# Kernel tuning notes

Hardware: AMD Instinct MI355X
Metric: run time of the kernel (lower is better)

Reference implementation:

```python
import jax, jax.numpy as jnp
import numpy as np

D_MODEL = 1024
N_HEADS = 16
D_K = D_MODEL // N_HEADS  # 64
D_V = D_MODEL // N_HEADS  # 64
BATCH = 2
SEQ = 2048


def setup_inputs() -> dict:
    key = jax.random.key(0)
    k_x, k_q, k_k, k_v, k_o = jax.random.split(key, 5)
    s = 1.0 / np.sqrt(D_MODEL)
    return {
        "X": jax.random.normal(k_x, (BATCH, SEQ, D_MODEL), dtype=jnp.float32),
        "W_Q": jax.random.normal(k_q, (D_MODEL, N_HEADS * D_K), dtype=jnp.float32) * s,
        "W_K": jax.random.normal(k_k, (D_MODEL, N_HEADS * D_K), dtype=jnp.float32) * s,
        "W_V": jax.random.normal(k_v, (D_MODEL, N_HEADS * D_V), dtype=jnp.float32) * s,
        "W_0": jax.random.normal(k_o, (N_HEADS * D_V, D_MODEL), dtype=jnp.float32) * s,
    }


def reference(X, W_Q, W_K, W_V, W_0):
    B, S, _ = X.shape
    # Project and split heads: [B, S, H, Dk]
    Q = (X @ W_Q).reshape(B, S, N_HEADS, D_K)
    K = (X @ W_K).reshape(B, S, N_HEADS, D_K)
    V = (X @ W_V).reshape(B, S, N_HEADS, D_V)
    # NOTE: original torch code scales by sqrt(K.shape[1]) == sqrt(seq_len),
    # not sqrt(d_k). Reproduce that exactly.
    scale = jnp.sqrt(jnp.asarray(S, dtype=X.dtype))
    scores = jnp.einsum("bqhd,bkhd->bhqk", Q, K) / scale  # [B, H, S, S]
    attn = jax.nn.softmax(scores, axis=-1)
    out = jnp.einsum("bhqk,bkhd->bqhd", attn, V)  # [B, S, H, Dv]
    return out.reshape(B, S, N_HEADS * D_V) @ W_0
```

## Files before the change

kernel.cpp:

```cpp
#include <hip/hip_runtime.h>

#define D_MODEL 1024
#define SEQ     2048
#define BATCH   2
#define NH      16

using u16 = unsigned short;
typedef __bf16 bf16x8 __attribute__((ext_vector_type(8)));
typedef float  f32x4  __attribute__((ext_vector_type(4)));

__device__ __forceinline__ u16 f2bf(float f){
  union { __bf16 h; u16 u; } v; v.h = (__bf16)f; return v.u;
}

__device__ __forceinline__ void gload_lds16(const void* g, void* l){
  __builtin_amdgcn_global_load_lds(
      (const __attribute__((address_space(1))) void*)g,
      (__attribute__((address_space(3))) void*)l, 16, 0, 0);
}

__global__ __launch_bounds__(256) void k_prep(
    const float* __restrict__ X, u16* __restrict__ Xb,
    const float* __restrict__ wq, const float* __restrict__ wk,
    const float* __restrict__ wv, const float* __restrict__ w0,
    u16* __restrict__ oq, u16* __restrict__ ok,
    u16* __restrict__ ov, u16* __restrict__ o0)
{
  const int t = threadIdx.x;
  if (blockIdx.x < 4096){
    int i = blockIdx.x*256 + t;
    float4 v = ((const float4*)X)[i];
    ushort4 o; o.x=f2bf(v.x); o.y=f2bf(v.y); o.z=f2bf(v.z); o.w=f2bf(v.w);
    ((ushort4*)Xb)[i] = o;
    return;
  }
  const int bid = blockIdx.x - 4096;
  const int z = bid >> 8, rem = bid & 255;
  const int nt = (rem & 15)*64, kt = (rem >> 4)*64;
  const float* W; u16* O;
  if      (z==0){W=wq;O=oq;}
  else if (z==1){W=wk;O=ok;}
  else if (z==2){W=wv;O=ov;}
  else          {W=w0;O=o0;}
  __shared__ float T[64][65];
  int r0 = t>>4, cb = (t&15)*4;
  #pragma unroll
  for (int j=0;j<4;++j){
    int r = r0 + j*16;
    float4 v = *(const float4*)(W + (size_t)(kt + r)*1024 + nt + cb);
    T[r][cb] = v.x; T[r][cb+1] = v.y; T[r][cb+2] = v.z; T[r][cb+3] = v.w;
  }
  __syncthreads();
  #pragma unroll
  for (int j=0;j<4;++j){
    int rn = r0 + j*16;
    ushort4 o;
    o.x = f2bf(T[cb  ][rn]); o.y = f2bf(T[cb+1][rn]);
    o.z = f2bf(T[cb+2][rn]); o.w = f2bf(T[cb+3][rn]);
    *(ushort4*)(O + (size_t)(nt + rn)*1024 + kt + cb) = o;
  }
}

__global__ __launch_bounds__(256) void k_gemm_qkv(
    const u16* __restrict__ A, const u16* __restrict__ Bt,
    u16* __restrict__ Ob, u16* __restrict__ Vt, float scaleQ)
{
  const int K = 1024, N = 3072;
  const int nwg = gridDim.x * gridDim.y;
  const int f = blockIdx.y * gridDim.x + blockIdx.x;
  const int sw = (f & 7) * (nwg >> 3) + (f >> 3);
  const int bxs = sw % gridDim.x, bys = sw / gridDim.x;
  const int bm = bys*128, bn = bxs*128;
  const float scl = (bn < 1024) ? scaleQ : 1.0f;
  const int lane = threadIdx.x & 63, w = threadIdx.x >> 6;
  const int hi = lane >> 4, c = lane & 15;
  const int wr = w >> 1, wc = w & 1;

  __shared__ u16 As[2][128*32];
  __shared__ u16 Bs[2][128*32];

  const int i0 = 2*w, i1 = 2*w+1;
  const int rA0 = i0*16 + (lane>>2), rA1 = i1*16 + (lane>>2);
  const int cA  = (lane&3)*8;
  const u16* aS0 = A  + (size_t)(bm + rA0)*K + cA;
  const u16* aS1 = A  + (size_t)(bm + rA1)*K + cA;
  const u16* bS0 = Bt + (size_t)(bn + rA0)*K + cA;
  const u16* bS1 = Bt + (size_t)(bn + rA1)*K + cA;

  auto stage = [&](int buf, int kk){
    gload_lds16(aS0 + kk, As[buf] + i0*512);
    gload_lds16(aS1 + kk, As[buf] + i1*512);
    gload_lds16(bS0 + kk, Bs[buf] + i0*512);
    gload_lds16(bS1 + kk, Bs[buf] + i1*512);
  };

  f32x4 acc[4][4];
  #pragma unroll
  for (int mi=0;mi<4;++mi)
    #pragma unroll
    for (int ni=0;ni<4;++ni) acc[mi][ni] = (f32x4){0.f,0.f,0.f,0.f};

  stage(0, 0);
  __syncthreads();
  int cur = 0;
  for (int kk = 0; kk < K; kk += 32){
    if (kk + 32 < K) stage(cur^1, kk + 32);
    const u16* as = As[cur];
    const u16* bs = Bs[cur];
    bf16x8 af[4], bfr[4];
    #pragma unroll
    for (int mi=0;mi<4;++mi)
      af[mi] = *(const bf16x8*)(as + (wr*64 + mi*16 + c)*32 + hi*8);
    #pragma unroll
    for (int ni=0;ni<4;++ni)
      bfr[ni] = *(const bf16x8*)(bs + (wc*64 + ni*16 + c)*32 + hi*8);
    #pragma unroll
    for (int mi=0;mi<4;++mi)
      #pragma unroll
      for (int ni=0;ni<4;++ni)
        acc[mi][ni] = __builtin_amdgcn_mfma_f32_16x16x32_bf16(af[mi], bfr[ni], acc[mi][ni], 0, 0, 0);
    __syncthreads();
    cur ^= 1;
  }

  if (bn < 2048){
    #pragma unroll
    for (int mi=0;mi<4;++mi){
      #pragma unroll
      for (int ni=0;ni<4;++ni){
        int row = bm + wr*64 + mi*16 + hi*4;
        int col = bn + wc*64 + ni*16 + c;
        #pragma unroll
        for (int r=0;r<4;++r)
          Ob[(size_t)(row + r)*N + col] = f2bf(acc[mi][ni][r] * scl);
      }
    }
  } else {
    #pragma unroll
    for (int mi=0;mi<4;++mi){
      int row = bm + wr*64 + mi*16 + hi*4;
      int b_  = row >> 11, s_ = row & 2047;
      int st  = s_ >> 6,  sl = s_ & 63;
      int p   = (sl & 0x23) | ((sl & 0x10) >> 2) | ((sl & 0x0C) << 1);
      #pragma unroll
      for (int ni=0;ni<4;++ni){
        int col = (bn - 2048) + wc*64 + ni*16 + c;
        int h_ = col >> 6, d_ = col & 63;
        u16* dst = Vt + ((size_t)(b_*16 + h_)*64 + d_)*SEQ + st*64 + p;
        ushort4 o;
        o.x = f2bf(acc[mi][ni][0]); o.y = f2bf(acc[mi][ni][1]);
        o.z = f2bf(acc[mi][ni][2]); o.w = f2bf(acc[mi][ni][3]);
        *(ushort4*)dst = o;
      }
    }
  }
}

__global__ __launch_bounds__(256) void k_gemm_out(
    const u16* __restrict__ A, const u16* __restrict__ Bt,
    float* __restrict__ OF)
{
  const int K = 1024, N = 1024;
  const int nwg = gridDim.x * gridDim.y;
  const int f = blockIdx.y * gridDim.x + blockIdx.x;
  const int sw = (f & 7) * (nwg >> 3) + (f >> 3);
  const int bxs = sw % gridDim.x, bys = sw / gridDim.x;
  const int bm = bys*128, bn = bxs*128;
  const int lane = threadIdx.x & 63, w = threadIdx.x >> 6;
  const int hi = lane >> 4, c = lane & 15;
  const int wr = w >> 1, wc = w & 1;

  __shared__ u16 As[2][128*32];
  __shared__ u16 Bs[2][128*32];

  const int i0 = 2*w, i1 = 2*w+1;
  const int rA0 = i0*16 + (lane>>2), rA1 = i1*16 + (lane>>2);
  const int cA  = (lane&3)*8;
  const u16* aS0 = A  + (size_t)(bm + rA0)*K + cA;
  const u16* aS1 = A  + (size_t)(bm + rA1)*K + cA;
  const u16* bS0 = Bt + (size_t)(bn + rA0)*K + cA;
  const u16* bS1 = Bt + (size_t)(bn + rA1)*K + cA;

  auto stage = [&](int buf, int kk){
    gload_lds16(aS0 + kk, As[buf] + i0*512);
    gload_lds16(aS1 + kk, As[buf] + i1*512);
    gload_lds16(bS0 + kk, Bs[buf] + i0*512);
    gload_lds16(bS1 + kk, Bs[buf] + i1*512);
  };

  f32x4 acc[4][4];
  #pragma unroll
  for (int mi=0;mi<4;++mi)
    #pragma unroll
    for (int ni=0;ni<4;++ni) acc[mi][ni] = (f32x4){0.f,0.f,0.f,0.f};

  stage(0, 0);
  __syncthreads();
  int cur = 0;
  for (int kk = 0; kk < K; kk += 32){
    if (kk + 32 < K) stage(cur^1, kk + 32);
    const u16* as = As[cur];
    const u16* bs = Bs[cur];
    bf16x8 af[4], bfr[4];
    #pragma unroll
    for (int mi=0;mi<4;++mi)
      af[mi] = *(const bf16x8*)(as + (wr*64 + mi*16 + c)*32 + hi*8);
    #pragma unroll
    for (int ni=0;ni<4;++ni)
      bfr[ni] = *(const bf16x8*)(bs + (wc*64 + ni*16 + c)*32 + hi*8);
    #pragma unroll
    for (int mi=0;mi<4;++mi)
      #pragma unroll
      for (int ni=0;ni<4;++ni)
        acc[mi][ni] = __builtin_amdgcn_mfma_f32_16x16x32_bf16(af[mi], bfr[ni], acc[mi][ni], 0, 0, 0);
    __syncthreads();
    cur ^= 1;
  }
  #pragma unroll
  for (int mi=0;mi<4;++mi){
    #pragma unroll
    for (int ni=0;ni<4;++ni){
      int row = bm + wr*64 + mi*16 + hi*4;
      int col = bn + wc*64 + ni*16 + c;
      #pragma unroll
      for (int r=0;r<4;++r)
        OF[(size_t)(row + r)*N + col] = acc[mi][ni][r];
    }
  }
}

__global__ __launch_bounds__(256, 2) void k_attn(const u16* __restrict__ QKV,
                                                 const u16* __restrict__ Vt,
                                                 u16* __restrict__ AO)
{
  const int bh = blockIdx.x, qt = blockIdx.y;
  const int b = bh >> 4, h = bh & 15;
  const int lane = threadIdx.x & 63, w = threadIdx.x >> 6;
  const int qg = w >> 1, kh = w & 1;
  const int hi = lane >> 4, c = lane & 15;

  __shared__ u16 Ks[2][64*64];
  __shared__ u16 Vs[2][64*64];

  const size_t qrow0 = (size_t)(b*SEQ + qt*128 + qg*64 + c);
  bf16x8 qf0[4], qf1[4];
  #pragma unroll
  for (int s=0;s<4;++s){
    qf0[s] = *(const bf16x8*)(QKV + (qrow0 + s*16)*3072 + h*64 + hi*8);
    qf1[s] = *(const bf16x8*)(QKV + (qrow0 + s*16)*3072 + h*64 + 32 + hi*8);
  }

  bf16x8 ones8;
  #pragma unroll
  for (int j=0;j<8;++j) ones8[j] = (__bf16)1.0f;

  f32x4 acc_o[4][4];
  f32x4 acc_l[4];
  #pragma unroll
  for (int s=0;s<4;++s){
    acc_l[s] = (f32x4){0.f,0.f,0.f,0.f};
    #pragma unroll
    for (int n=0;n<4;++n) acc_o[s][n] = (f32x4){0.f,0.f,0.f,0.f};
  }

  const int r0 = w*8 + (lane>>3);
  const int r1 = 32 + r0;
  const int sb = ((((lane&7)*16) ^ ((lane>>3)<<4)) >> 1);
  const u16* kS0 = QKV + (size_t)(b*SEQ + r0)*3072 + 1024 + h*64 + sb;
  const u16* kS1 = QKV + (size_t)(b*SEQ + r1)*3072 + 1024 + h*64 + sb;
  const u16* vS0 = Vt + ((size_t)bh*64 + r0)*SEQ + sb;
  const u16* vS1 = Vt + ((size_t)bh*64 + r1)*SEQ + sb;

  auto stage = [&](int buf){
    gload_lds16(kS0, Ks[buf] + w*512);
    gload_lds16(kS1, Ks[buf] + 2048 + w*512);
    gload_lds16(vS0, Vs[buf] + w*512);
    gload_lds16(vS1, Vs[buf] + 2048 + w*512);
    kS0 += (size_t)64*3072; kS1 += (size_t)64*3072; vS0 += 64; vS1 += 64;
  };

  const int swz = ((c&7)<<4);
  const char* kr0 = (const char*)&Ks[0][0] + (kh*32 + c)*128 + (( 0 + hi*16) ^ swz);
  const char* kr1 = (const char*)&Ks[0][0] + (kh*32 + c)*128 + ((64 + hi*16) ^ swz);
  const char* vr  = (const char*)&Vs[0][0] + c*128 + ((kh*64 + hi*16) ^ swz);

  auto body = [&](int buf){
    const int bo = buf*8192;
    bf16x8 k00 = *(const bf16x8*)(kr0 + bo);
    bf16x8 k01 = *(const bf16x8*)(kr1 + bo);
    bf16x8 k10 = *(const bf16x8*)(kr0 + bo + 2048);
    bf16x8 k11 = *(const bf16x8*)(kr1 + bo + 2048);
    bf16x8 vv0 = *(const bf16x8*)(vr + bo);
    bf16x8 vv1 = *(const bf16x8*)(vr + bo + 2048);
    bf16x8 vv2 = *(const bf16x8*)(vr + bo + 4096);
    bf16x8 vv3 = *(const bf16x8*)(vr + bo + 6144);
    #pragma unroll
    for (int s=0;s<4;++s){
      f32x4 s0 = (f32x4){0.f,0.f,0.f,0.f};
      f32x4 s1 = (f32x4){0.f,0.f,0.f,0.f};
      __builtin_amdgcn_s_setprio(1);
      s0 = __builtin_amdgcn_mfma_f32_16x16x32_bf16(k00, qf0[s], s0, 0,0,0);
      s1 = __builtin_amdgcn_mfma_f32_16x16x32_bf16(k10, qf0[s], s1, 0,0,0);
      s0 = __builtin_amdgcn_mfma_f32_16x16x32_bf16(k01, qf1[s], s0, 0,0,0);
      s1 = __builtin_amdgcn_mfma_f32_16x16x32_bf16(k11, qf1[s], s1, 0,0,0);
      __builtin_amdgcn_s_setprio(0);
      bf16x8 a;
      #pragma unroll
      for (int i=0;i<4;++i){
        a[i]   = (__bf16)__builtin_amdgcn_exp2f(s0[i]);
        a[i+4] = (__bf16)__builtin_amdgcn_exp2f(s1[i]);
      }
      __builtin_amdgcn_s_setprio(1);
      acc_l[s]    = __builtin_amdgcn_mfma_f32_16x16x32_bf16(a, ones8, acc_l[s], 0,0,0);
      acc_o[s][0] = __builtin_amdgcn_mfma_f32_16x16x32_bf16(a, vv0, acc_o[s][0], 0,0,0);
      acc_o[s][1] = __builtin_amdgcn_mfma_f32_16x16x32_bf16(a, vv1, acc_o[s][1], 0,0,0);
      acc_o[s][2] = __builtin_amdgcn_mfma_f32_16x16x32_bf16(a, vv2, acc_o[s][2], 0,0,0);
      acc_o[s][3] = __builtin_amdgcn_mfma_f32_16x16x32_bf16(a, vv3, acc_o[s][3], 0,0,0);
      __builtin_amdgcn_s_setprio(0);
    }
  };

  stage(0);
  __syncthreads();
  #pragma unroll 1
  for (int u = 0; u < SEQ/128; ++u){
    stage(1);
    body(0);
    __syncthreads();
    if (u != SEQ/128 - 1) stage(0);
    body(1);
    __syncthreads();
  }

  float* Of = (float*)&Ks[0][0];
  float* Lf = (float*)&Vs[0][0];
  #pragma unroll
  for (int s=0;s<4;++s){
    if (kh == 1){
      #pragma unroll
      for (int n=0;n<4;++n)
        #pragma unroll
        for (int i=0;i<4;++i)
          Of[qg*1024 + (hi*4+i)*64 + n*16 + c] = acc_o[s][n][i];
      if (c == 0){
        #pragma unroll
        for (int i=0;i<4;++i) Lf[qg*16 + hi*4 + i] = acc_l[s][i];
      }
    }
    __syncthreads();
    if (kh == 0){
      float inv[4];
      #pragma unroll
      for (int i=0;i<4;++i)
        inv[i] = 1.0f / (acc_l[s][i] + Lf[qg*16 + hi*4 + i]);
      size_t obase = (size_t)(b*SEQ + qt*128 + qg*64 + s*16 + hi*4)*D_MODEL + h*64;
      #pragma unroll
      for (int i=0;i<4;++i){
        #pragma unroll
        for (int n=0;n<4;++n){
          float o = acc_o[s][n][i] + Of[qg*1024 + (hi*4+i)*64 + n*16 + c];
          AO[obase + (size_t)i*D_MODEL + n*16 + c] = f2bf(o * inv[i]);
        }
      }
    }
    __syncthreads();
  }
}

extern "C" void kernel_launch(void* const* d_in, const int* in_sizes, int n_in,
                              void* d_out, int out_size, void* d_ws, size_t ws_size,
                              hipStream_t stream)
{
  const float* X  = (const float*)d_in[0];
  const float* Wq = (const float*)d_in[1];
  const float* Wk = (const float*)d_in[2];
  const float* Wv = (const float*)d_in[3];
  const float* W0 = (const float*)d_in[4];
  float* out = (float*)d_out;

  char* ws = (char*)d_ws;
  const size_t MB = 1024*1024;
  u16* Xb    = (u16*)(ws);
  u16* WqkvT = (u16*)(ws +  8*MB);
  u16* W0T   = (u16*)(ws + 14*MB);
  u16* QKVb  = (u16*)(ws + 16*MB);
  u16* Vt    = (u16*)(ws + 40*MB);
  u16* AO    = Xb;

  const float scaleQ = 1.4426950408889634f / sqrtf((float)SEQ);
  const int M = BATCH*SEQ;

  k_prep<<<dim3(4096 + 1024), 256, 0, stream>>>(
      X, Xb, Wq, Wk, Wv, W0,
      WqkvT, WqkvT + 1024*1024, WqkvT + 2*1024*1024, W0T);
  k_gemm_qkv<<<dim3(3072/128, M/128), 256, 0, stream>>>(
      Xb, WqkvT, QKVb, Vt, scaleQ);
  k_attn<<<dim3(BATCH*NH, SEQ/128), 256, 0, stream>>>(QKVb, Vt, AO);
  k_gemm_out<<<dim3(1024/128, M/128), 256, 0, stream>>>(AO, W0T, out);
}
```

Baseline: 104.7 us.

## Load K/V tiles directly into registers instead of staging through LDS

The attention kernel drops the double-buffered LDS staging of K and V tiles, where global_load_lds was followed by swizzled LDS reads and barriers. Each wave now loads its K and V fragments straight from global memory into registers, ping-ponging between two register sets, so the main loop needs no __syncthreads. This removes LDS traffic and barrier stalls, but each K/V tile is now fetched by several waves through the caches instead of once per block. It also removes the min-2-blocks occupancy hint from launch bounds, which lets the compiler use more registers.

```diff
diff --git a/kernel.cpp b/kernel.cpp
--- a/kernel.cpp
+++ b/kernel.cpp
@@ -229,9 +229,9 @@
   }
 }
 
-__global__ __launch_bounds__(256, 2) void k_attn(const u16* __restrict__ QKV,
-                                                 const u16* __restrict__ Vt,
-                                                 u16* __restrict__ AO)
+__global__ __launch_bounds__(256) void k_attn(const u16* __restrict__ QKV,
+                                              const u16* __restrict__ Vt,
+                                              u16* __restrict__ AO)
 {
   const int bh = blockIdx.x, qt = blockIdx.y;
   const int b = bh >> 4, h = bh & 15;
@@ -239,8 +239,8 @@
   const int qg = w >> 1, kh = w & 1;
   const int hi = lane >> 4, c = lane & 15;
 
-  __shared__ u16 Ks[2][64*64];
-  __shared__ u16 Vs[2][64*64];
+  __shared__ float Of[2][1024];
+  __shared__ float Lf[2][16];
 
   const size_t qrow0 = (size_t)(b*SEQ + qt*128 + qg*64 + c);
   bf16x8 qf0[4], qf1[4];
@@ -263,46 +263,31 @@
     for (int n=0;n<4;++n) acc_o[s][n] = (f32x4){0.f,0.f,0.f,0.f};
   }
 
-  const int r0 = w*8 + (lane>>3);
-  const int r1 = 32 + r0;
-  const int sb = ((((lane&7)*16) ^ ((lane>>3)<<4)) >> 1);
-  const u16* kS0 = QKV + (size_t)(b*SEQ + r0)*3072 + 1024 + h*64 + sb;
-  const u16* kS1 = QKV + (size_t)(b*SEQ + r1)*3072 + 1024 + h*64 + sb;
-  const u16* vS0 = Vt + ((size_t)bh*64 + r0)*SEQ + sb;
-  const u16* vS1 = Vt + ((size_t)bh*64 + r1)*SEQ + sb;
-
-  auto stage = [&](int buf){
-    gload_lds16(kS0, Ks[buf] + w*512);
-    gload_lds16(kS1, Ks[buf] + 2048 + w*512);
-    gload_lds16(vS0, Vs[buf] + w*512);
-    gload_lds16(vS1, Vs[buf] + 2048 + w*512);
-    kS0 += (size_t)64*3072; kS1 += (size_t)64*3072; vS0 += 64; vS1 += 64;
-  };
-
-  const int swz = ((c&7)<<4);
-  const char* kr0 = (const char*)&Ks[0][0] + (kh*32 + c)*128 + (( 0 + hi*16) ^ swz);
-  const char* kr1 = (const char*)&Ks[0][0] + (kh*32 + c)*128 + ((64 + hi*16) ^ swz);
-  const char* vr  = (const char*)&Vs[0][0] + c*128 + ((kh*64 + hi*16) ^ swz);
-
-  auto body = [&](int buf){
-    const int bo = buf*8192;
-    bf16x8 k00 = *(const bf16x8*)(kr0 + bo);
-    bf16x8 k01 = *(const bf16x8*)(kr1 + bo);
-    bf16x8 k10 = *(const bf16x8*)(kr0 + bo + 2048);
-    bf16x8 k11 = *(const bf16x8*)(kr1 + bo + 2048);
-    bf16x8 vv0 = *(const bf16x8*)(vr + bo);
-    bf16x8 vv1 = *(const bf16x8*)(vr + bo + 2048);
-    bf16x8 vv2 = *(const bf16x8*)(vr + bo + 4096);
-    bf16x8 vv3 = *(const bf16x8*)(vr + bo + 6144);
+  const u16* kb = QKV + (size_t)(b*SEQ + kh*32 + c)*3072 + 1024 + h*64 + hi*8;
+  const u16* vb = Vt + ((size_t)bh*64 + c)*SEQ + kh*32 + hi*8;
+
+  auto loadK = [&](const u16* p, bf16x8* K4){
+    K4[0] = *(const bf16x8*)(p);
+    K4[1] = *(const bf16x8*)(p + 32);
+    K4[2] = *(const bf16x8*)(p + 16*3072);
+    K4[3] = *(const bf16x8*)(p + 16*3072 + 32);
+  };
+  auto loadV = [&](const u16* p, bf16x8* V4){
+    V4[0] = *(const bf16x8*)(p);
+    V4[1] = *(const bf16x8*)(p + 16*SEQ);
+    V4[2] = *(const bf16x8*)(p + 32*SEQ);
+    V4[3] = *(const bf16x8*)(p + 48*SEQ);
+  };
+  auto compute = [&](const bf16x8* K4, const bf16x8* V4){
     #pragma unroll
     for (int s=0;s<4;++s){
       f32x4 s0 = (f32x4){0.f,0.f,0.f,0.f};
       f32x4 s1 = (f32x4){0.f,0.f,0.f,0.f};
       __builtin_amdgcn_s_setprio(1);
-      s0 = __builtin_amdgcn_mfma_f32_16x16x32_bf16(k00, qf0[s], s0, 0,0,0);
-      s1 = __builtin_amdgcn_mfma_f32_16x16x32_bf16(k10, qf0[s], s1, 0,0,0);
-      s0 = __builtin_amdgcn_mfma_f32_16x16x32_bf16(k01, qf1[s], s0, 0,0,0);
-      s1 = __builtin_amdgcn_mfma_f32_16x16x32_bf16(k11, qf1[s], s1, 0,0,0);
+      s0 = __builtin_amdgcn_mfma_f32_16x16x32_bf16(K4[0], qf0[s], s0, 0,0,0);
+      s1 = __builtin_amdgcn_mfma_f32_16x16x32_bf16(K4[2], qf0[s], s1, 0,0,0);
+      s0 = __builtin_amdgcn_mfma_f32_16x16x32_bf16(K4[1], qf1[s], s0, 0,0,0);
+      s1 = __builtin_amdgcn_mfma_f32_16x16x32_bf16(K4[3], qf1[s], s1, 0,0,0);
       __builtin_amdgcn_s_setprio(0);
       bf16x8 a;
       #pragma unroll
@@ -312,28 +297,29 @@
       }
       __builtin_amdgcn_s_setprio(1);
       acc_l[s]    = __builtin_amdgcn_mfma_f32_16x16x32_bf16(a, ones8, acc_l[s], 0,0,0);
-      acc_o[s][0] = __builtin_amdgcn_mfma_f32_16x16x32_bf16(a, vv0, acc_o[s][0], 0,0,0);
-      acc_o[s][1] = __builtin_amdgcn_mfma_f32_16x16x32_bf16(a, vv1, acc_o[s][1], 0,0,0);
-      acc_o[s][2] = __builtin_amdgcn_mfma_f32_16x16x32_bf16(a, vv2, acc_o[s][2], 0,0,0);
-      acc_o[s][3] = __builtin_amdgcn_mfma_f32_16x16x32_bf16(a, vv3, acc_o[s][3], 0,0,0);
+      acc_o[s][0] = __builtin_amdgcn_mfma_f32_16x16x32_bf16(a, V4[0], acc_o[s][0], 0,0,0);
+      acc_o[s][1] = __builtin_amdgcn_mfma_f32_16x16x32_bf16(a, V4[1], acc_o[s][1], 0,0,0);
+      acc_o[s][2] = __builtin_amdgcn_mfma_f32_16x16x32_bf16(a, V4[2], acc_o[s][2], 0,0,0);
+      acc_o[s][3] = __builtin_amdgcn_mfma_f32_16x16x32_bf16(a, V4[3], acc_o[s][3], 0,0,0);
       __builtin_amdgcn_s_setprio(0);
     }
   };
 
-  stage(0);
-  __syncthreads();
+  bf16x8 kA[4], vA[4], kB[4], vB[4];
+  loadK(kb, kA); loadV(vb, vA);
+  kb += (size_t)64*3072; vb += 64;
   #pragma unroll 1
-  for (int u = 0; u < SEQ/128; ++u){
-    stage(1);
-    body(0);
-    __syncthreads();
-    if (u != SEQ/128 - 1) stage(0);
-    body(1);
-    __syncthreads();
-  }
-
-  float* Of = (float*)&Ks[0][0];
-  float* Lf = (float*)&Vs[0][0];
+  for (int u = 0; u < 32; u += 2){
+    loadK(kb, kB); loadV(vb, vB);
+    kb += (size_t)64*3072; vb += 64;
+    compute(kA, vA);
+    if (u + 2 < 32){
+      loadK(kb, kA); loadV(vb, vA);
+      kb += (size_t)64*3072; vb += 64;
+    }
+    compute(kB, vB);
+  }
+
   #pragma unroll
   for (int s=0;s<4;++s){
     if (kh == 1){
@@ -341,10 +327,10 @@
       for (int n=0;n<4;++n)
         #pragma unroll
         for (int i=0;i<4;++i)
-          Of[qg*1024 + (hi*4+i)*64 + n*16 + c] = acc_o[s][n][i];
+          Of[qg][(hi*4+i)*64 + n*16 + c] = acc_o[s][n][i];
       if (c == 0){
         #pragma unroll
-        for (int i=0;i<4;++i) Lf[qg*16 + hi*4 + i] = acc_l[s][i];
+        for (int i=0;i<4;++i) Lf[qg][hi*4 + i] = acc_l[s][i];
       }
     }
     __syncthreads();
@@ -352,13 +338,13 @@
       float inv[4];
       #pragma unroll
       for (int i=0;i<4;++i)
-        inv[i] = 1.0f / (acc_l[s][i] + Lf[qg*16 + hi*4 + i]);
+        inv[i] = 1.0f / (acc_l[s][i] + Lf[qg][hi*4 + i]);
       size_t obase = (size_t)(b*SEQ + qt*128 + qg*64 + s*16 + hi*4)*D_MODEL + h*64;
       #pragma unroll
       for (int i=0;i<4;++i){
         #pragma unroll
         for (int n=0;n<4;++n){
-          float o = acc_o[s][n][i] + Of[qg*1024 + (hi*4+i)*64 + n*16 + c];
+          float o = acc_o[s][n][i] + Of[qg][(hi*4+i)*64 + n*16 + c];
           AO[obase + (size_t)i*D_MODEL + n*16 + c] = f2bf(o * inv[i]);
         }
       }
```

Result: slower. 134.6 us (+28.5%).
